# Performance work log

Measured on AMD Instinct MI355X. Metric: run time of the kernel, lower is better.

Reference implementation:

```python
import jax, jax.numpy as jnp
import numpy as np

ORDER = 2            # spline order kx = ky
H = W = 7            # control_grid_dims
KSZ = 3.0            # kernel_size -> bbox = (-1.5, 1.5)
OUT, IN = 32, 32     # out_channels, in_groups (groups=1)
N = 32768            # number of query points
BBOX = KSZ / 2.0


def _make_knots(n_coef, lo, hi, order):
    # clamped knot vector of length n_coef + order + 1 (as scipy produces)
    n_interior = n_coef - order - 1
    interior = np.linspace(lo, hi, n_interior + 2)[1:-1]
    t = np.concatenate([[lo] * (order + 1), interior, [hi] * (order + 1)])
    return jnp.asarray(t, dtype=jnp.float32)


def setup_inputs() -> dict:
    key = jax.random.key(0)
    k1, k2 = jax.random.split(key)
    # query points strictly inside the bbox
    xy = jax.random.uniform(k1, (N, 2), dtype=jnp.float32,
                            minval=-BBOX * 0.95, maxval=BBOX * 0.95)
    # control coefficients C: [out_channels, in_groups, h, w]
    C = jax.random.normal(k2, (OUT, IN, H, W), dtype=jnp.float32) * 0.1
    Tx = _make_knots(H, -BBOX, BBOX, ORDER)
    Ty = _make_knots(W, -BBOX, BBOX, ORDER)
    return {"xy": xy, "Tx": Tx, "Ty": Ty, "C": C}


def _find_span(T, v, p):
    # torch: (T <= v).min(dim=-1) -> first False index, minus 1; if all True -> len(T)-p-2
    ss = jnp.searchsorted(T, v, side="right")          # number of knots <= v
    return jnp.where(ss == T.shape[0], T.shape[0] - p - 2, ss - 1)


def _safe_div(num, den):
    return num / jnp.where(den == 0, jnp.ones_like(den), den)


def reference(xy, Tx, Ty, C):
    px = py = ORDER
    X = xy[:, 0]
    Y = xy[:, 1]
    kx = _find_span(Tx, X, px)   # [N] knot spans
    ky = _find_span(Ty, Y, py)

    dim = OUT * IN
    Ctrl = C.reshape(dim, H, W)
    offs = jnp.arange(px + 1)
    ix = kx[:, None] - px + offs                 # [N, px+1]
    iy = ky[:, None] - py + offs                 # [N, py+1]
    # gather local (px+1)x(py+1) control patch per point: [N, Dim, px+1, py+1]
    D = Ctrl[:, ix[:, :, None], iy[:, None, :]]
    D = jnp.transpose(D, (1, 0, 2, 3))

    rng = jnp.arange(px)
    # de Boor recursion along x
    for r in range(1, px + 1):
        t_lo = Tx[kx[:, None] - px + 1 + rng]    # [N, px]
        t_hi = Tx[kx[:, None] + 2 - r + rng]
        alphax = _safe_div(X[:, None] - t_lo, t_hi - t_lo)
        for j in range(px, r - 1, -1):
            a = alphax[:, j - 1][:, None, None]
            D = D.at[:, :, j, :].set((1 - a) * D[:, :, j - 1, :] + a * D[:, :, j, :])
    # de Boor recursion along y (on the collapsed x row px)
    for r in range(1, py + 1):
        t_lo = Ty[ky[:, None] - py + 1 + rng]
        t_hi = Ty[ky[:, None] + 2 - r + rng]
        alphay = _safe_div(Y[:, None] - t_lo, t_hi - t_lo)
        for j in range(py, r - 1, -1):
            a = alphay[:, j - 1][:, None]
            D = D.at[:, :, px, j].set((1 - a) * D[:, :, px, j - 1] + a * D[:, :, px, j])

    return D[:, :, px, py].reshape(xy.shape[0], OUT, IN)
```

## Files before the change

### kernel.cpp

```cpp
#include <hip/hip_runtime.h>


#define NPTS   32768
#define DIM    1024
#define PPB    64
#define RSTR   12

__device__ __forceinline__ float safe_div(float n, float d) {
    return (d == 0.0f) ? n : (n / d);
}

__device__ __forceinline__ void span_weights(float v, const float* __restrict__ T,
                                             int& k, float& w0, float& w1, float& w2) {
    float t3 = T[3], t4 = T[4], t5 = T[5], t6 = T[6];
    k = 2 + (v >= t3) + (v >= t4) + (v >= t5) + (v >= t6);
    float Tm1 = T[k - 1], T0 = T[k], Tp1 = T[k + 1], Tp2 = T[k + 2];
    float a10 = safe_div(v - Tm1, Tp1 - Tm1);
    float a11 = safe_div(v - T0,  Tp2 - T0);
    float a21 = safe_div(v - T0,  Tp1 - T0);
    w0 = (1.0f - a21) * (1.0f - a10);
    w1 = (1.0f - a21) * a10 + a21 * (1.0f - a11);
    w2 = a21 * a11;
}

__global__ __launch_bounds__(256) void spline_main_kernel(
    const float* __restrict__ C,
    const float* __restrict__ xy,
    const float* __restrict__ Tx,
    const float* __restrict__ Ty,
    float* __restrict__ out)
{
    __shared__ float recs[PPB][RSTR];

    const int t     = threadIdx.x;
    const int g     = blockIdx.x & 1;
    const int chunk = blockIdx.x >> 1;
    const int p0    = chunk * PPB;
    const int ch    = g * 512 + t * 2;

    if (t < PPB) {
        const int p = p0 + t;
        const float2 pt = ((const float2*)xy)[p];
        int kx, ky;
        float wx0, wx1, wx2, wy0, wy1, wy2;
        span_weights(pt.x, Tx, kx, wx0, wx1, wx2);
        span_weights(pt.y, Ty, ky, wy0, wy1, wy2);
        float* r = recs[t];
        r[0] = wx0 * wy0;  r[1] = wx0 * wy1;  r[2] = wx0 * wy2;
        r[3] = wx1 * wy0;  r[4] = wx1 * wy1;  r[5] = wx1 * wy2;
        r[6] = wx2 * wy0;  r[7] = wx2 * wy1;  r[8] = wx2 * wy2;
        r[9] = __int_as_float((kx - 2) * 7 + (ky - 2));
        r[10] = 0.0f; r[11] = 0.0f;
    }

    float c[98];
    {
        const float2* src = (const float2*)(C + (size_t)ch * 49);
#pragma unroll
        for (int q = 0; q < 49; ++q) {
            float2 v = src[q];
            c[2 * q]     = v.x;
            c[2 * q + 1] = v.y;
        }
    }

    __syncthreads();

    float2* outp = (float2*)(out + (size_t)p0 * DIM + ch);

    float4 wA = *(const float4*)(&recs[0][0]);
    float4 wB = *(const float4*)(&recs[0][4]);
    float2 wC = *(const float2*)(&recs[0][8]);

    for (int i = 0; i < PPB; ++i) {
        const float w0 = wA.x, w1 = wA.y, w2 = wA.z, w3 = wA.w;
        const float w4 = wB.x, w5 = wB.y, w6 = wB.z, w7 = wB.w;
        const float w8 = wC.x;
        const int off = __builtin_amdgcn_readfirstlane(__float_as_int(wC.y));

        if (i + 1 < PPB) {
            wA = *(const float4*)(&recs[i + 1][0]);
            wB = *(const float4*)(&recs[i + 1][4]);
            wC = *(const float2*)(&recs[i + 1][8]);
        }

        float s0, s1;
        switch (off) {
#define TERM(q, dq, w)                                      \
            s0 = fmaf(w, c[(q) + (dq)],      s0);           \
            s1 = fmaf(w, c[49 + (q) + (dq)], s1);
#define CASE_IJ(i_, j_)                                     \
        case ((i_) * 7 + (j_)): {                           \
            const int q = (i_) * 7 + (j_);                  \
            s0 = w0 * c[q];                                 \
            s1 = w0 * c[49 + q];                            \
            TERM(q, 1,  w1)  TERM(q, 2,  w2)                \
            TERM(q, 7,  w3)  TERM(q, 8,  w4)  TERM(q, 9,  w5) \
            TERM(q, 14, w6)  TERM(q, 15, w7)  TERM(q, 16, w8) \
        } break;
        CASE_IJ(0, 0) CASE_IJ(0, 1) CASE_IJ(0, 2) CASE_IJ(0, 3) CASE_IJ(0, 4)
        CASE_IJ(1, 0) CASE_IJ(1, 1) CASE_IJ(1, 2) CASE_IJ(1, 3) CASE_IJ(1, 4)
        CASE_IJ(2, 0) CASE_IJ(2, 1) CASE_IJ(2, 2) CASE_IJ(2, 3) CASE_IJ(2, 4)
        CASE_IJ(3, 0) CASE_IJ(3, 1) CASE_IJ(3, 2) CASE_IJ(3, 3) CASE_IJ(3, 4)
        CASE_IJ(4, 0) CASE_IJ(4, 1) CASE_IJ(4, 2) CASE_IJ(4, 3) CASE_IJ(4, 4)
#undef CASE_IJ
#undef TERM
        default: s0 = 0.0f; s1 = 0.0f; break;
        }

        *outp = make_float2(s0, s1);
        outp += DIM / 2;
    }
}

extern "C" void kernel_launch(void* const* d_in, const int* in_sizes, int n_in,
                              void* d_out, int out_size, void* d_ws, size_t ws_size,
                              hipStream_t stream) {
    const float* xy = (const float*)d_in[0];
    const float* Tx = (const float*)d_in[1];
    const float* Ty = (const float*)d_in[2];
    const float* C  = (const float*)d_in[3];
    float* out = (float*)d_out;

    spline_main_kernel<<<2 * (NPTS / PPB), 256, 0, stream>>>(C, xy, Tx, Ty, out);
}
```

Baseline: 38.43 us.

## Split weight/coeff prep into separate kernel and transpose C for coalesced loads

Adds a prep kernel that computes the per-point spline weights and patch offsets into workspace and transposes the control coefficients to a [49][DIM] layout. The main kernel then uses 512-thread blocks covering all 1024 channels, loads coefficients with coalesced reads, double-buffers weight records read from global memory instead of shared memory, and writes output with nontemporal stores. This removes redundant per-block weight computation, the block-level barrier and the strided coefficient loads. In exchange it adds a second launch plus a workspace round trip, and the 98-float register array under launch_bounds(512,4) may pressure registers.

Measured after the change: 50.95 us. +32.6%, slower.

```diff
diff --git a/kernel.cpp b/kernel.cpp
--- a/kernel.cpp
+++ b/kernel.cpp
@@ -5,6 +5,9 @@
 #define DIM    1024
 #define PPB    64
 #define RSTR   12
+#define NRECB  128
+
+typedef float f32x2 __attribute__((ext_vector_type(2)));
 
 __device__ __forceinline__ float safe_div(float n, float d) {
     return (d == 0.0f) ? n : (n / d);
@@ -23,69 +26,89 @@
     w2 = a21 * a11;
 }
 
-__global__ __launch_bounds__(256) void spline_main_kernel(
-    const float* __restrict__ C,
+__global__ __launch_bounds__(256) void prep_kernel(
     const float* __restrict__ xy,
     const float* __restrict__ Tx,
     const float* __restrict__ Ty,
-    float* __restrict__ out)
+    const float* __restrict__ C,
+    float* __restrict__ wts,
+    float* __restrict__ CT)
 {
-    __shared__ float recs[PPB][RSTR];
-
-    const int t     = threadIdx.x;
-    const int g     = blockIdx.x & 1;
-    const int chunk = blockIdx.x >> 1;
-    const int p0    = chunk * PPB;
-    const int ch    = g * 512 + t * 2;
-
-    if (t < PPB) {
-        const int p = p0 + t;
-        const float2 pt = ((const float2*)xy)[p];
+    const int b = blockIdx.x;
+    const int t = threadIdx.x;
+    if (b < NRECB) {
+        const int n = b * 256 + t;
+        const float2 pt = ((const float2*)xy)[n];
         int kx, ky;
         float wx0, wx1, wx2, wy0, wy1, wy2;
         span_weights(pt.x, Tx, kx, wx0, wx1, wx2);
         span_weights(pt.y, Ty, ky, wy0, wy1, wy2);
-        float* r = recs[t];
+        float* r = wts + (size_t)n * RSTR;
         r[0] = wx0 * wy0;  r[1] = wx0 * wy1;  r[2] = wx0 * wy2;
         r[3] = wx1 * wy0;  r[4] = wx1 * wy1;  r[5] = wx1 * wy2;
         r[6] = wx2 * wy0;  r[7] = wx2 * wy1;  r[8] = wx2 * wy2;
         r[9] = __int_as_float((kx - 2) * 7 + (ky - 2));
         r[10] = 0.0f; r[11] = 0.0f;
+    } else {
+        const int ch = (b - NRECB) * 256 + t;
+#pragma unroll
+        for (int q = 0; q < 49; ++q)
+            CT[q * DIM + ch] = C[(size_t)ch * 49 + q];
+    }
+}
+
+__global__ __launch_bounds__(512, 4) void spline_main_kernel(
+    const float* __restrict__ CT,
+    const float* __restrict__ wts,
+    float* __restrict__ out)
+{
+    const int t  = threadIdx.x;
+    const int p0 = blockIdx.x * PPB;
+
+    float c[98];
+#pragma unroll
+    for (int q = 0; q < 49; ++q) {
+        f32x2 v = *(const f32x2*)(CT + q * DIM + 2 * t);
+        c[q]      = v.x;
+        c[49 + q] = v.y;
     }
 
-    float c[98];
-    {
-        const float2* src = (const float2*)(C + (size_t)ch * 49);
-#pragma unroll
-        for (int q = 0; q < 49; ++q) {
-            float2 v = src[q];
-            c[2 * q]     = v.x;
-            c[2 * q + 1] = v.y;
-        }
+    f32x2* outp = (f32x2*)(out + (size_t)p0 * DIM + 2 * t);
+    const float* wp = wts + (size_t)p0 * RSTR;
+
+    float4 aA = *(const float4*)(wp + 0);
+    float4 aB = *(const float4*)(wp + 4);
+    float2 aC = *(const float2*)(wp + 8);
+    float4 bA = *(const float4*)(wp + RSTR + 0);
+    float4 bB = *(const float4*)(wp + RSTR + 4);
+    float2 bC = *(const float2*)(wp + RSTR + 8);
+
+#define BODY(WA, WB, WC, PF_IDX)                                        \
+    {                                                                   \
+        const int off = __builtin_amdgcn_readfirstlane(__float_as_int((WC).y)); \
+        const float w0 = (WA).x, w1 = (WA).y, w2 = (WA).z, w3 = (WA).w; \
+        const float w4 = (WB).x, w5 = (WB).y, w6 = (WB).z, w7 = (WB).w; \
+        const float w8 = (WC).x;                                        \
+        {       \
+            const int j = (PF_IDX) < PPB ? (PF_IDX) : (PPB - 1);        \
+            (WA) = *(const float4*)(wp + (size_t)j * RSTR + 0);         \
+            (WB) = *(const float4*)(wp + (size_t)j * RSTR + 4);         \
+            (WC) = *(const float2*)(wp + (size_t)j * RSTR + 8);         \
+        }                                                               \
+        float s0, s1;                                                   \
+        switch (off) {                                                  \
+        CASE_IJ(0, 0) CASE_IJ(0, 1) CASE_IJ(0, 2) CASE_IJ(0, 3) CASE_IJ(0, 4) \
+        CASE_IJ(1, 0) CASE_IJ(1, 1) CASE_IJ(1, 2) CASE_IJ(1, 3) CASE_IJ(1, 4) \
+        CASE_IJ(2, 0) CASE_IJ(2, 1) CASE_IJ(2, 2) CASE_IJ(2, 3) CASE_IJ(2, 4) \
+        CASE_IJ(3, 0) CASE_IJ(3, 1) CASE_IJ(3, 2) CASE_IJ(3, 3) CASE_IJ(3, 4) \
+        CASE_IJ(4, 0) CASE_IJ(4, 1) CASE_IJ(4, 2) CASE_IJ(4, 3) CASE_IJ(4, 4) \
+        default: s0 = 0.0f; s1 = 0.0f; break;                           \
+        }                                                               \
+        f32x2 v2; v2.x = s0; v2.y = s1;                                 \
+        __builtin_nontemporal_store(v2, outp);                          \
+        outp += DIM / 2;                                                \
     }
 
-    __syncthreads();
-
-    float2* outp = (float2*)(out + (size_t)p0 * DIM + ch);
-
-    float4 wA = *(const float4*)(&recs[0][0]);
-    float4 wB = *(const float4*)(&recs[0][4]);
-    float2 wC = *(const float2*)(&recs[0][8]);
-
-    for (int i = 0; i < PPB; ++i) {
-        const float w0 = wA.x, w1 = wA.y, w2 = wA.z, w3 = wA.w;
-        const float w4 = wB.x, w5 = wB.y, w6 = wB.z, w7 = wB.w;
-        const float w8 = wC.x;
-        const int off = __builtin_amdgcn_readfirstlane(__float_as_int(wC.y));
-
-        if (i + 1 < PPB) {
-            wA = *(const float4*)(&recs[i + 1][0]);
-            wB = *(const float4*)(&recs[i + 1][4]);
-            wC = *(const float2*)(&recs[i + 1][8]);
-        }
-
-        float s0, s1;
-        switch (off) {
 #define TERM(q, dq, w)                                      \
             s0 = fmaf(w, c[(q) + (dq)],      s0);           \
             s1 = fmaf(w, c[49 + (q) + (dq)], s1);
@@ -98,19 +121,15 @@
             TERM(q, 7,  w3)  TERM(q, 8,  w4)  TERM(q, 9,  w5) \
             TERM(q, 14, w6)  TERM(q, 15, w7)  TERM(q, 16, w8) \
         } break;
-        CASE_IJ(0, 0) CASE_IJ(0, 1) CASE_IJ(0, 2) CASE_IJ(0, 3) CASE_IJ(0, 4)
-        CASE_IJ(1, 0) CASE_IJ(1, 1) CASE_IJ(1, 2) CASE_IJ(1, 3) CASE_IJ(1, 4)
-        CASE_IJ(2, 0) CASE_IJ(2, 1) CASE_IJ(2, 2) CASE_IJ(2, 3) CASE_IJ(2, 4)
-        CASE_IJ(3, 0) CASE_IJ(3, 1) CASE_IJ(3, 2) CASE_IJ(3, 3) CASE_IJ(3, 4)
-        CASE_IJ(4, 0) CASE_IJ(4, 1) CASE_IJ(4, 2) CASE_IJ(4, 3) CASE_IJ(4, 4)
+
+    for (int i = 0; i < PPB; i += 2) {
+        BODY(aA, aB, aC, i + 2)
+        BODY(bA, bB, bC, i + 3)
+    }
+
 #undef CASE_IJ
 #undef TERM
-        default: s0 = 0.0f; s1 = 0.0f; break;
-        }
-
-        *outp = make_float2(s0, s1);
-        outp += DIM / 2;
-    }
+#undef BODY
 }
 
 extern "C" void kernel_launch(void* const* d_in, const int* in_sizes, int n_in,
@@ -122,5 +141,9 @@
     const float* C  = (const float*)d_in[3];
     float* out = (float*)d_out;
 
-    spline_main_kernel<<<2 * (NPTS / PPB), 256, 0, stream>>>(C, xy, Tx, Ty, out);
+    float* CT  = (float*)d_ws;
+    float* wts = CT + 49 * DIM;
+
+    prep_kernel<<<NRECB + DIM / 256, 256, 0, stream>>>(xy, Tx, Ty, C, wts, CT);
+    spline_main_kernel<<<NPTS / PPB, 512, 0, stream>>>(CT, wts, out);
 }
```
